# Kernel optimization log

Measured on AMD Instinct MI355X. Metric: run time of the kernel, lower is better.

The kernel has to match this reference:

```python
import jax, jax.numpy as jnp
import numpy as np

EPS = 1e-5
NUM_GROUPS = 32

def _nin(x, w, b):
    # 1x1 conv: x (B,C,H,W), w (K,C), b (K,)
    return jnp.einsum('bchw,kc->bkhw', x, w) + b[None, :, None, None]

def _group_norm(x, gamma, beta, num_groups=NUM_GROUPS, eps=EPS):
    B, C, H, W = x.shape
    xg = x.reshape(B, num_groups, C // num_groups, H, W)
    mean = xg.mean(axis=(2, 3, 4), keepdims=True)
    var = xg.var(axis=(2, 3, 4), keepdims=True)
    xg = (xg - mean) * jax.lax.rsqrt(var + eps)
    x = xg.reshape(B, C, H, W)
    return x * gamma[None, :, None, None] + beta[None, :, None, None]

def setup_inputs() -> dict:
    key = jax.random.key(0)
    ks = jax.random.split(key, 10)
    B, C, H, W = 8, 512, 64, 64
    att = 512
    s = 0.02
    return {
        'x': jax.random.normal(ks[0], (B, C, H, W), dtype=jnp.float32),
        'gn_weight': jnp.ones((C,), jnp.float32),
        'gn_bias': jnp.zeros((C,), jnp.float32),
        'q_w': jax.random.normal(ks[1], (att, C), jnp.float32) * s,
        'q_b': jnp.zeros((att,), jnp.float32),
        'k_w': jax.random.normal(ks[2], (att, C), jnp.float32) * s,
        'k_b': jnp.zeros((att,), jnp.float32),
        'v_w': jax.random.normal(ks[3], (att, C), jnp.float32) * s,
        'v_b': jnp.zeros((att,), jnp.float32),
        'proj_w': jax.random.normal(ks[4], (C, att), jnp.float32) * s,
        'proj_b': jnp.zeros((C,), jnp.float32),
    }

def reference(x, gn_weight, gn_bias, q_w, q_b, k_w, k_b, v_w, v_b, proj_w, proj_b):
    B, C, H, W = x.shape
    h = _group_norm(x, gn_weight, gn_bias)
    q = _nin(h, q_w, q_b)  # (B, D, H, W)
    k = _nin(h, k_w, k_b)
    v = _nin(h, v_w, v_b)
    N = H * W
    qf = q.reshape(B, -1, N)
    kf = k.reshape(B, -1, N)
    vf = v.reshape(B, -1, N)
    scale = C ** (-0.5)  # note: scaled by input channel C, per source
    w = jnp.einsum('bdn,bdm->bnm', qf, kf) * scale  # (B, N, N)
    w = jax.nn.softmax(w, axis=-1)
    hf = jnp.einsum('bnm,bdm->bdn', w, vf)
    h = hf.reshape(B, -1, H, W)
    h = _nin(h, proj_w, proj_b)
    return x + h
```

## Files before the change

kernel.cpp:

```cpp
#include <hip/hip_runtime.h>
#include <hip/hip_bf16.h>
#include <cstdint>
#include <cstddef>

typedef __bf16 bf16_t;
typedef __bf16 bf16x8 __attribute__((ext_vector_type(8)));
typedef __bf16 bf16x4 __attribute__((ext_vector_type(4)));
typedef float f32x4 __attribute__((ext_vector_type(4)));

__device__ __forceinline__ void async16(const void* g, void* l) {
  __builtin_amdgcn_global_load_lds(
      (const __attribute__((address_space(1))) void*)g,
      (__attribute__((address_space(3))) void*)l,
      16, 0, 0);
}

__global__ __launch_bounds__(256) void f2b4(const float* __restrict__ w0,
                                            const float* __restrict__ w1,
                                            const float* __restrict__ w2,
                                            const float* __restrict__ w3,
                                            bf16_t* __restrict__ o0,
                                            bf16_t* __restrict__ o1,
                                            bf16_t* __restrict__ o2,
                                            bf16_t* __restrict__ o3) {
  const float* in = (blockIdx.y == 0) ? w0 : (blockIdx.y == 1) ? w1
                   : (blockIdx.y == 2) ? w2 : w3;
  bf16_t* out = (blockIdx.y == 0) ? o0 : (blockIdx.y == 1) ? o1
               : (blockIdx.y == 2) ? o2 : o3;
  const int i = blockIdx.x * 256 + threadIdx.x;
  float4 v = ((const float4*)in)[i];
  bf16x4 o = { (__bf16)v.x, (__bf16)v.y, (__bf16)v.z, (__bf16)v.w };
  ((bf16x4*)out)[i] = o;
}

__global__ __launch_bounds__(256) void groupnorm_t(const float* __restrict__ x,
                                                   const float* __restrict__ gamma,
                                                   const float* __restrict__ beta,
                                                   bf16_t* __restrict__ ht) {
  const int g = blockIdx.x;
  const int b = blockIdx.y;
  const int t = threadIdx.x;
  const float* xg = x + ((size_t)(b * 512 + g * 16)) * 4096;
  const float4* x4 = (const float4*)xg;

  float s = 0.f, ss = 0.f;
  #pragma unroll 8
  for (int i = t; i < 16384; i += 256) {
    float4 v = x4[i];
    s  += (v.x + v.y) + (v.z + v.w);
    ss += (v.x * v.x + v.y * v.y) + (v.z * v.z + v.w * v.w);
  }
  #pragma unroll
  for (int o = 32; o; o >>= 1) { s += __shfl_xor(s, o); ss += __shfl_xor(ss, o); }
  __shared__ float rs[4], rss[4];
  if ((t & 63) == 0) { rs[t >> 6] = s; rss[t >> 6] = ss; }
  __syncthreads();
  const float S  = (rs[0] + rs[1]) + (rs[2] + rs[3]);
  const float SS = (rss[0] + rss[1]) + (rss[2] + rss[3]);
  const float inv_n = 1.0f / 65536.0f;
  const float mean = S * inv_n;
  const float var  = SS * inv_n - mean * mean;
  const float rstd = rsqrtf(var + 1e-5f);

  float ga[16], be[16];
  #pragma unroll
  for (int cc = 0; cc < 16; cc++) {
    const float gm = gamma[g * 16 + cc] * rstd;
    ga[cc] = gm;
    be[cc] = beta[g * 16 + cc] - mean * gm;
  }

  bf16_t* hg = ht + (size_t)b * 4096 * 512 + g * 16;
  for (int n = t; n < 4096; n += 256) {
    bf16_t o[16];
    #pragma unroll
    for (int cc = 0; cc < 16; cc++)
      o[cc] = (bf16_t)(xg[(size_t)cc * 4096 + n] * ga[cc] + be[cc]);
    bf16x8* dst = (bf16x8*)(hg + (size_t)n * 512);
    dst[0] = *(bf16x8*)&o[0];
    dst[1] = *(bf16x8*)&o[8];
  }
}

template <int OUTF32, int BIAS_MODE, int RESID, int SWAP>
__global__ __launch_bounds__(256)
void gemm_bt(const bf16_t* __restrict__ A, const bf16_t* __restrict__ B,
             void* __restrict__ Cv, const float* __restrict__ bias,
             const float* __restrict__ resid,
             int TM, int TN, int Z, int K, float scale,
             long sA, long sB, long sC, long sR) {
  __shared__ alignas(16) bf16_t lA[4096];
  __shared__ alignas(16) bf16_t lB[4096];

  const int lid = blockIdx.x;
  const int xcd = lid & 7;
  const int j   = lid >> 3;
  const int sd  = SWAP ? TN : TM;
  const int I   = SWAP ? TM : TN;
  const int spx = (sd * Z) >> 3;
  const int strip = xcd * spx + j / I;
  const int inner = j % I;
  const int z    = strip / sd;
  const int sidx = strip % sd;
  const int bm = (SWAP ? inner : sidx) * 128;
  const int bn = (SWAP ? sidx : inner) * 128;
  const int N = TN * 128;

  const int t = threadIdx.x;
  const int lane = t & 63;
  const int w = t >> 6;
  const int wm = (w >> 1) * 64;
  const int wn = (w & 1) * 64;
  const bf16_t* Ab = A + (size_t)z * (size_t)sA;
  const bf16_t* Bb = B + (size_t)z * (size_t)sB;

  const int lrow = lane >> 2;
  const int lcol = (lane & 3) * 8;
  const int quad = lane >> 4;
  const int l15 = lane & 15;

  const bf16_t* gA0 = Ab + (size_t)(bm + w * 16 + lrow) * K + lcol;
  const bf16_t* gA1 = Ab + (size_t)(bm + (w + 4) * 16 + lrow) * K + lcol;
  const bf16_t* gB0 = Bb + (size_t)(bn + w * 16 + lrow) * K + lcol;
  const bf16_t* gB1 = Bb + (size_t)(bn + (w + 4) * 16 + lrow) * K + lcol;
  bf16_t* lA0 = &lA[w * 512];
  bf16_t* lA1 = &lA[(w + 4) * 512];
  bf16_t* lB0 = &lB[w * 512];
  bf16_t* lB1 = &lB[(w + 4) * 512];

  f32x4 acc[4][4] = {};

  for (int k0 = 0; k0 < K; k0 += 32) {
    __syncthreads();
    async16(gA0 + k0, lA0);
    async16(gA1 + k0, lA1);
    async16(gB0 + k0, lB0);
    async16(gB1 + k0, lB1);
    __syncthreads();

    bf16x8 af[4], bfr[4];
    #pragma unroll
    for (int i = 0; i < 4; i++) {
      af[i]  = *(const bf16x8*)&lA[(wm + i * 16 + l15) * 32 + quad * 8];
      bfr[i] = *(const bf16x8*)&lB[(wn + i * 16 + l15) * 32 + quad * 8];
    }
    #pragma unroll
    for (int i = 0; i < 4; i++)
      #pragma unroll
      for (int jj = 0; jj < 4; jj++)
        acc[i][jj] = __builtin_amdgcn_mfma_f32_16x16x32_bf16(af[i], bfr[jj],
                                                             acc[i][jj], 0, 0, 0);
  }

  float* Cf = (float*)Cv + (size_t)z * (size_t)sC;
  bf16_t* Cb = (bf16_t*)Cv + (size_t)z * (size_t)sC;
  const float* Rb = RESID ? (resid + (size_t)z * (size_t)sR) : nullptr;

  #pragma unroll
  for (int i = 0; i < 4; i++) {
    const int row0 = bm + wm + i * 16 + quad * 4;
    #pragma unroll
    for (int jj = 0; jj < 4; jj++) {
      const int col = bn + wn + jj * 16 + l15;
      #pragma unroll
      for (int r = 0; r < 4; r++) {
        float v = acc[i][jj][r] * scale;
        const int row = row0 + r;
        if (BIAS_MODE == 1) v += bias[row];
        else if (BIAS_MODE == 2) v += bias[col];
        const size_t idx = (size_t)row * N + col;
        if (RESID) v += Rb[idx];
        if (OUTF32) Cf[idx] = v;
        else Cb[idx] = (bf16_t)v;
      }
    }
  }
}

__global__ __launch_bounds__(256, 2)
void flash_attn(const bf16_t* __restrict__ Qm, const bf16_t* __restrict__ Km,
                const bf16_t* __restrict__ Vm, bf16_t* __restrict__ Om,
                float scale) {
  __shared__ alignas(16) bf16_t lT[4][128][32];
  __shared__ alignas(16) bf16_t lS[4][16][144];

  const int bid = blockIdx.x;
  const int z = bid & 7;
  const int qb = bid >> 3;
  const int m0 = qb * 64;

  const int t = threadIdx.x;
  const int lane = t & 63;
  const int w = t >> 6;
  const int quad = lane >> 4;
  const int l15 = lane & 15;
  const int srow = lane >> 2;
  const int scol = (lane & 3) * 8;

  const size_t sND = 4096ull * 512;
  const bf16_t* q = Qm + z * sND;
  const bf16_t* k = Km + z * sND;
  const bf16_t* v = Vm + z * sND;

  bf16x8 qf[16];
  {
    const bf16_t* qrow = q + (size_t)(m0 + w * 16 + l15) * 512 + quad * 8;
    #pragma unroll
    for (int kk = 0; kk < 16; kk++)
      qf[kk] = *(const bf16x8*)(qrow + kk * 32);
  }

  f32x4 o_acc[32] = {};
  float l_run[4] = {0.f, 0.f, 0.f, 0.f};

  for (int kc = 0; kc < 4096; kc += 128) {
    f32x4 s_acc[8] = {};
    #pragma unroll
    for (int kd2 = 0; kd2 < 4; kd2++) {
      __syncthreads();
      #pragma unroll
      for (int c = 0; c < 8; c++) {
        const int p = c >> 1;
        const int keyblk = w * 32 + (c & 1) * 16;
        const bf16_t* g = k + (size_t)(kc + keyblk + srow) * 512
                            + kd2 * 128 + p * 32 + scol;
        async16(g, &lT[p][keyblk][0] + srow * 32 + scol);
      }
      __syncthreads();
      #pragma unroll
      for (int p = 0; p < 4; p++)
        #pragma unroll
        for (int n = 0; n < 8; n++) {
          bf16x8 kf = *(const bf16x8*)&lT[p][n * 16 + l15][quad * 8];
          s_acc[n] = __builtin_amdgcn_mfma_f32_16x16x32_bf16(
              qf[kd2 * 4 + p], kf, s_acc[n], 0, 0, 0);
        }
    }

    float lsum[4] = {0.f, 0.f, 0.f, 0.f};
    #pragma unroll
    for (int n = 0; n < 8; n++)
      #pragma unroll
      for (int r = 0; r < 4; r++) {
        float e = __expf(s_acc[n][r] * scale);
        lsum[r] += e;
        lS[w][quad * 4 + r][n * 16 + l15] = (bf16_t)e;
      }
    #pragma unroll
    for (int r = 0; r < 4; r++) {
      float s = lsum[r];
      s += __shfl_xor(s, 1); s += __shfl_xor(s, 2);
      s += __shfl_xor(s, 4); s += __shfl_xor(s, 8);
      l_run[r] += s;
    }

    #pragma unroll
    for (int db = 0; db < 4; db++) {
      __syncthreads();
      #pragma unroll
      for (int c = 0; c < 8; c++) {
        const int p = c >> 1;
        const int dblk = w * 32 + (c & 1) * 16;
        const bf16_t* g = v + (size_t)(db * 128 + dblk + srow) * 4096
                            + kc + p * 32 + scol;
        async16(g, &lT[p][dblk][0] + srow * 32 + scol);
      }
      __syncthreads();
      #pragma unroll
      for (int p = 0; p < 4; p++) {
        bf16x8 af = *(const bf16x8*)&lS[w][l15][p * 32 + quad * 8];
        #pragma unroll
        for (int nd = 0; nd < 8; nd++) {
          bf16x8 vf = *(const bf16x8*)&lT[p][nd * 16 + l15][quad * 8];
          o_acc[db * 8 + nd] = __builtin_amdgcn_mfma_f32_16x16x32_bf16(
              af, vf, o_acc[db * 8 + nd], 0, 0, 0);
        }
      }
    }
  }

  bf16_t* o = Om + z * sND;
  float rl[4];
  #pragma unroll
  for (int r = 0; r < 4; r++) rl[r] = 1.0f / l_run[r];
  #pragma unroll
  for (int nd = 0; nd < 32; nd++)
    #pragma unroll
    for (int r = 0; r < 4; r++) {
      const int row = m0 + w * 16 + quad * 4 + r;
      const int col = nd * 16 + l15;
      o[(size_t)row * 512 + col] = (bf16_t)(o_acc[nd][r] * rl[r]);
    }
}

extern "C" void kernel_launch(void* const* d_in, const int* in_sizes, int n_in,
                              void* d_out, int out_size, void* d_ws, size_t ws_size,
                              hipStream_t stream) {
  const float* x   = (const float*)d_in[0];
  const float* gnw = (const float*)d_in[1];
  const float* gnb = (const float*)d_in[2];
  const float* qw  = (const float*)d_in[3];
  const float* qb  = (const float*)d_in[4];
  const float* kw  = (const float*)d_in[5];
  const float* kb  = (const float*)d_in[6];
  const float* vw  = (const float*)d_in[7];
  const float* vb  = (const float*)d_in[8];
  const float* pw  = (const float*)d_in[9];
  const float* pb  = (const float*)d_in[10];
  float* out = (float*)d_out;

  char* ws = (char*)d_ws;
  size_t off = 0;
  auto alloc = [&](size_t bytes) -> void* {
    void* p = ws + off;
    off += (bytes + 255) & ~(size_t)255;
    return p;
  };

  const long sND = 4096L * 512;

  bf16_t* wqb = (bf16_t*)alloc(512ull * 512 * 2);
  bf16_t* wkb = (bf16_t*)alloc(512ull * 512 * 2);
  bf16_t* wvb = (bf16_t*)alloc(512ull * 512 * 2);
  bf16_t* wpb = (bf16_t*)alloc(512ull * 512 * 2);
  bf16_t* ht  = (bf16_t*)alloc(8ull * 4096 * 512 * 2);
  bf16_t* qbf = (bf16_t*)alloc(8ull * 4096 * 512 * 2);
  bf16_t* kbf = (bf16_t*)alloc(8ull * 4096 * 512 * 2);
  bf16_t* vbf = (bf16_t*)alloc(8ull * 4096 * 512 * 2);
  bf16_t* hfb = ht;

  f2b4<<<dim3(256, 4), 256, 0, stream>>>(qw, kw, vw, pw, wqb, wkb, wvb, wpb);
  groupnorm_t<<<dim3(32, 8), 256, 0, stream>>>(x, gnw, gnb, ht);

  gemm_bt<0, 2, 0, 0><<<1024, 256, 0, stream>>>(
      ht, wqb, qbf, qb, nullptr, 32, 4, 8, 512, 1.0f, sND, 0, sND, 0);
  gemm_bt<0, 2, 0, 0><<<1024, 256, 0, stream>>>(
      ht, wkb, kbf, kb, nullptr, 32, 4, 8, 512, 1.0f, sND, 0, sND, 0);
  gemm_bt<0, 1, 0, 1><<<1024, 256, 0, stream>>>(
      wvb, ht, vbf, vb, nullptr, 4, 32, 8, 512, 1.0f, 0, sND, sND, 0);

  const float scale = 0.044194173824159216f;
  flash_attn<<<512, 256, 0, stream>>>(qbf, kbf, vbf, hfb, scale);

  gemm_bt<1, 1, 1, 1><<<1024, 256, 0, stream>>>(
      wpb, hfb, out, pb, x, 4, 32, 8, 512, 1.0f, 0, sND, 512L * 4096, 512L * 4096);
}
```

Measured before the change: 747.5 us.

## Double-buffer K/V tiles in flash attention with prefetch and swizzled LDS

Replaces the single LDS tile, which was loaded and then waited on before every MMA step, with a two-slot buffer. The next K or V slab is prefetched with async global-to-LDS loads while the current slab is consumed, and the prefetch continues across the K-to-V and V-to-next-K boundaries. It also stores tiles in fragment-native order so each lane reads contiguously, XOR-swizzles the probability tile to avoid bank conflicts, and raises wave priority around the MMA loops. The cost is twice the LDS footprint, which may reduce occupancy.

```diff
diff --git a/kernel.cpp b/kernel.cpp
--- a/kernel.cpp
+++ b/kernel.cpp
@@ -181,8 +181,8 @@
 void flash_attn(const bf16_t* __restrict__ Qm, const bf16_t* __restrict__ Km,
                 const bf16_t* __restrict__ Vm, bf16_t* __restrict__ Om,
                 float scale) {
-  __shared__ alignas(16) bf16_t lT[4][128][32];
-  __shared__ alignas(16) bf16_t lS[4][16][144];
+  __shared__ alignas(16) bf16_t lK[2][16384];
+  __shared__ alignas(16) bf16_t lS[4][2048];
 
   const int bid = blockIdx.x;
   const int z = bid & 7;
@@ -194,14 +194,15 @@
   const int w = t >> 6;
   const int quad = lane >> 4;
   const int l15 = lane & 15;
-  const int srow = lane >> 2;
-  const int scol = (lane & 3) * 8;
 
   const size_t sND = 4096ull * 512;
   const bf16_t* q = Qm + z * sND;
   const bf16_t* k = Km + z * sND;
   const bf16_t* v = Vm + z * sND;
 
+  const int kOffK = l15 * 512 + quad * 8;
+  const int kOffV = l15 * 4096 + quad * 8;
+
   bf16x8 qf[16];
   {
     const bf16_t* qrow = q + (size_t)(m0 + w * 16 + l15) * 512 + quad * 8;
@@ -213,69 +214,102 @@
   f32x4 o_acc[32] = {};
   float l_run[4] = {0.f, 0.f, 0.f, 0.f};
 
+  #pragma unroll
+  for (int c = 0; c < 8; c++) {
+    const int p = c >> 1, n = (w << 1) | (c & 1);
+    async16(k + (size_t)(n * 16) * 512 + p * 32 + kOffK,
+            &lK[0][(p * 8 + n) << 9]);
+  }
+  __syncthreads();
+
   for (int kc = 0; kc < 4096; kc += 128) {
     f32x4 s_acc[8] = {};
+    float lsum[4] = {0.f, 0.f, 0.f, 0.f};
+
     #pragma unroll
     for (int kd2 = 0; kd2 < 4; kd2++) {
-      __syncthreads();
-      #pragma unroll
-      for (int c = 0; c < 8; c++) {
-        const int p = c >> 1;
-        const int keyblk = w * 32 + (c & 1) * 16;
-        const bf16_t* g = k + (size_t)(kc + keyblk + srow) * 512
-                            + kd2 * 128 + p * 32 + scol;
-        async16(g, &lT[p][keyblk][0] + srow * 32 + scol);
-      }
-      __syncthreads();
+      if (kd2 < 3) {
+        #pragma unroll
+        for (int c = 0; c < 8; c++) {
+          const int p = c >> 1, n = (w << 1) | (c & 1);
+          async16(k + (size_t)(kc + n * 16) * 512 + (kd2 + 1) * 128 + p * 32 + kOffK,
+                  &lK[(kd2 + 1) & 1][(p * 8 + n) << 9]);
+        }
+      } else {
+        #pragma unroll
+        for (int c = 0; c < 8; c++) {
+          const int p = c >> 1, nd = (w << 1) | (c & 1);
+          async16(v + (size_t)(nd * 16) * 4096 + kc + p * 32 + kOffV,
+                  &lK[(kd2 + 1) & 1][(p * 8 + nd) << 9]);
+        }
+      }
+      const bf16_t* buf = lK[kd2 & 1];
+      __builtin_amdgcn_s_setprio(1);
       #pragma unroll
       for (int p = 0; p < 4; p++)
         #pragma unroll
         for (int n = 0; n < 8; n++) {
-          bf16x8 kf = *(const bf16x8*)&lT[p][n * 16 + l15][quad * 8];
+          bf16x8 kf = *(const bf16x8*)&buf[((p * 8 + n) << 9) + lane * 8];
           s_acc[n] = __builtin_amdgcn_mfma_f32_16x16x32_bf16(
               qf[kd2 * 4 + p], kf, s_acc[n], 0, 0, 0);
         }
-    }
-
-    float lsum[4] = {0.f, 0.f, 0.f, 0.f};
-    #pragma unroll
-    for (int n = 0; n < 8; n++)
-      #pragma unroll
-      for (int r = 0; r < 4; r++) {
-        float e = __expf(s_acc[n][r] * scale);
-        lsum[r] += e;
-        lS[w][quad * 4 + r][n * 16 + l15] = (bf16_t)e;
-      }
-    #pragma unroll
-    for (int r = 0; r < 4; r++) {
-      float s = lsum[r];
-      s += __shfl_xor(s, 1); s += __shfl_xor(s, 2);
-      s += __shfl_xor(s, 4); s += __shfl_xor(s, 8);
-      l_run[r] += s;
+      __builtin_amdgcn_s_setprio(0);
+
+      if (kd2 == 3) {
+        #pragma unroll
+        for (int n = 0; n < 8; n++)
+          #pragma unroll
+          for (int r = 0; r < 4; r++) {
+            float e = __expf(s_acc[n][r] * scale);
+            lsum[r] += e;
+            const int row = quad * 4 + r;
+            const int sl = ((n * 2 + (l15 >> 3)) ^ row) & 15;
+            lS[w][row * 128 + sl * 8 + (l15 & 7)] = (bf16_t)e;
+          }
+        #pragma unroll
+        for (int r = 0; r < 4; r++) {
+          float s = lsum[r];
+          s += __shfl_xor(s, 1); s += __shfl_xor(s, 2);
+          s += __shfl_xor(s, 4); s += __shfl_xor(s, 8);
+          l_run[r] += s;
+        }
+      }
+      __syncthreads();
     }
 
     #pragma unroll
     for (int db = 0; db < 4; db++) {
-      __syncthreads();
-      #pragma unroll
-      for (int c = 0; c < 8; c++) {
-        const int p = c >> 1;
-        const int dblk = w * 32 + (c & 1) * 16;
-        const bf16_t* g = v + (size_t)(db * 128 + dblk + srow) * 4096
-                            + kc + p * 32 + scol;
-        async16(g, &lT[p][dblk][0] + srow * 32 + scol);
-      }
-      __syncthreads();
+      if (db < 3) {
+        #pragma unroll
+        for (int c = 0; c < 8; c++) {
+          const int p = c >> 1, nd = (w << 1) | (c & 1);
+          async16(v + (size_t)((db + 1) * 128 + nd * 16) * 4096 + kc + p * 32 + kOffV,
+                  &lK[(db + 1) & 1][(p * 8 + nd) << 9]);
+        }
+      } else {
+        const int kc2 = (kc + 128) & 4095;
+        #pragma unroll
+        for (int c = 0; c < 8; c++) {
+          const int p = c >> 1, n = (w << 1) | (c & 1);
+          async16(k + (size_t)(kc2 + n * 16) * 512 + p * 32 + kOffK,
+                  &lK[(db + 1) & 1][(p * 8 + n) << 9]);
+        }
+      }
+      const bf16_t* buf = lK[db & 1];
+      __builtin_amdgcn_s_setprio(1);
       #pragma unroll
       for (int p = 0; p < 4; p++) {
-        bf16x8 af = *(const bf16x8*)&lS[w][l15][p * 32 + quad * 8];
+        bf16x8 af = *(const bf16x8*)
+            &lS[w][l15 * 128 + (((p * 4 + quad) ^ l15) & 15) * 8];
         #pragma unroll
         for (int nd = 0; nd < 8; nd++) {
-          bf16x8 vf = *(const bf16x8*)&lT[p][nd * 16 + l15][quad * 8];
+          bf16x8 vf = *(const bf16x8*)&buf[((p * 8 + nd) << 9) + lane * 8];
           o_acc[db * 8 + nd] = __builtin_amdgcn_mfma_f32_16x16x32_bf16(
               af, vf, o_acc[db * 8 + nd], 0, 0, 0);
         }
       }
+      __builtin_amdgcn_s_setprio(0);
+      __syncthreads();
     }
   }
 
```

After: 958.9 us. +28.3%, slower.

## Store K/V tiles in MFMA fragment order, swizzle P buffer, raise MFMA priority

Applied to the files above, without the earlier changes.

Rewrites the LDS layout of the K and V tiles so each async 16-byte load lands exactly where a lane later reads its MFMA operand, making the LDS reads contiguous per lane and free of bank conflicts. Adds an XOR swizzle to the probability (P) scratch buffer to remove bank conflicts on its writes and reads. Wraps the MFMA loops in s_setprio so compute waves get scheduling priority. The global load pattern changes to per-lane rows of 16 bytes, which may coalesce less well across lanes.

```diff
diff --git a/kernel.cpp b/kernel.cpp
--- a/kernel.cpp
+++ b/kernel.cpp
@@ -181,8 +181,8 @@
 void flash_attn(const bf16_t* __restrict__ Qm, const bf16_t* __restrict__ Km,
                 const bf16_t* __restrict__ Vm, bf16_t* __restrict__ Om,
                 float scale) {
-  __shared__ alignas(16) bf16_t lT[4][128][32];
-  __shared__ alignas(16) bf16_t lS[4][16][144];
+  __shared__ alignas(16) bf16_t lT[32][512];
+  __shared__ alignas(16) bf16_t lS[4][2048];
 
   const int bid = blockIdx.x;
   const int z = bid & 7;
@@ -194,14 +194,15 @@
   const int w = t >> 6;
   const int quad = lane >> 4;
   const int l15 = lane & 15;
-  const int srow = lane >> 2;
-  const int scol = (lane & 3) * 8;
 
   const size_t sND = 4096ull * 512;
   const bf16_t* q = Qm + z * sND;
   const bf16_t* k = Km + z * sND;
   const bf16_t* v = Vm + z * sND;
 
+  const int kOffK = l15 * 512 + quad * 8;
+  const int kOffV = l15 * 4096 + quad * 8;
+
   bf16x8 qf[16];
   {
     const bf16_t* qrow = q + (size_t)(m0 + w * 16 + l15) * 512 + quad * 8;
@@ -221,20 +222,21 @@
       #pragma unroll
       for (int c = 0; c < 8; c++) {
         const int p = c >> 1;
-        const int keyblk = w * 32 + (c & 1) * 16;
-        const bf16_t* g = k + (size_t)(kc + keyblk + srow) * 512
-                            + kd2 * 128 + p * 32 + scol;
-        async16(g, &lT[p][keyblk][0] + srow * 32 + scol);
+        const int n = (w << 1) | (c & 1);
+        async16(k + (size_t)(kc + n * 16) * 512 + kd2 * 128 + p * 32 + kOffK,
+                &lT[p * 8 + n][0]);
       }
       __syncthreads();
+      __builtin_amdgcn_s_setprio(1);
       #pragma unroll
       for (int p = 0; p < 4; p++)
         #pragma unroll
         for (int n = 0; n < 8; n++) {
-          bf16x8 kf = *(const bf16x8*)&lT[p][n * 16 + l15][quad * 8];
+          bf16x8 kf = *(const bf16x8*)&lT[p * 8 + n][lane * 8];
           s_acc[n] = __builtin_amdgcn_mfma_f32_16x16x32_bf16(
               qf[kd2 * 4 + p], kf, s_acc[n], 0, 0, 0);
         }
+      __builtin_amdgcn_s_setprio(0);
     }
 
     float lsum[4] = {0.f, 0.f, 0.f, 0.f};
@@ -244,7 +246,9 @@
       for (int r = 0; r < 4; r++) {
         float e = __expf(s_acc[n][r] * scale);
         lsum[r] += e;
-        lS[w][quad * 4 + r][n * 16 + l15] = (bf16_t)e;
+        const int row = quad * 4 + r;
+        const int sl = ((n * 2 + (l15 >> 3)) ^ row) & 15;
+        lS[w][row * 128 + sl * 8 + (l15 & 7)] = (bf16_t)e;
       }
     #pragma unroll
     for (int r = 0; r < 4; r++) {
@@ -260,22 +264,24 @@
       #pragma unroll
       for (int c = 0; c < 8; c++) {
         const int p = c >> 1;
-        const int dblk = w * 32 + (c & 1) * 16;
-        const bf16_t* g = v + (size_t)(db * 128 + dblk + srow) * 4096
-                            + kc + p * 32 + scol;
-        async16(g, &lT[p][dblk][0] + srow * 32 + scol);
+        const int nd = (w << 1) | (c & 1);
+        async16(v + (size_t)(db * 128 + nd * 16) * 4096 + kc + p * 32 + kOffV,
+                &lT[p * 8 + nd][0]);
       }
       __syncthreads();
+      __builtin_amdgcn_s_setprio(1);
       #pragma unroll
       for (int p = 0; p < 4; p++) {
-        bf16x8 af = *(const bf16x8*)&lS[w][l15][p * 32 + quad * 8];
+        bf16x8 af = *(const bf16x8*)
+            &lS[w][l15 * 128 + (((p * 4 + quad) ^ l15) & 15) * 8];
         #pragma unroll
         for (int nd = 0; nd < 8; nd++) {
-          bf16x8 vf = *(const bf16x8*)&lT[p][nd * 16 + l15][quad * 8];
+          bf16x8 vf = *(const bf16x8*)&lT[p * 8 + nd][lane * 8];
           o_acc[db * 8 + nd] = __builtin_amdgcn_mfma_f32_16x16x32_bf16(
               af, vf, o_acc[db * 8 + nd], 0, 0, 0);
         }
       }
+      __builtin_amdgcn_s_setprio(0);
     }
   }
 
```

Result: slower. 890.7 us (+19.2%).

## Double-buffer K/V staging and widen flash attention blocks to 8 waves

Applied to the files above, without the earlier changes.

Flash attention now uses 512-thread blocks covering 128 query rows, so each staged K/V tile in shared memory is shared by twice as many waves. K and V tiles are double-buffered: the next tile's async global-to-LDS load is issued before the MFMA work on the current buffer, leaving one barrier per stage instead of two. This is meant to hide load latency and cut global traffic per query. In exchange it uses more LDS per block and fewer blocks in total (256), which may affect occupancy and load balance across CUs.

```diff
diff --git a/kernel.cpp b/kernel.cpp
--- a/kernel.cpp
+++ b/kernel.cpp
@@ -177,17 +177,17 @@
   }
 }
 
-__global__ __launch_bounds__(256, 2)
+__global__ __launch_bounds__(512, 2)
 void flash_attn(const bf16_t* __restrict__ Qm, const bf16_t* __restrict__ Km,
                 const bf16_t* __restrict__ Vm, bf16_t* __restrict__ Om,
                 float scale) {
-  __shared__ alignas(16) bf16_t lT[4][128][32];
-  __shared__ alignas(16) bf16_t lS[4][16][144];
+  __shared__ alignas(16) bf16_t lT[2][4][128][32];
+  __shared__ alignas(16) bf16_t lS[8][16][144];
 
   const int bid = blockIdx.x;
   const int z = bid & 7;
   const int qb = bid >> 3;
-  const int m0 = qb * 64;
+  const int m0 = qb * 128;
 
   const int t = threadIdx.x;
   const int lane = t & 63;
@@ -202,6 +202,9 @@
   const bf16_t* k = Km + z * sND;
   const bf16_t* v = Vm + z * sND;
 
+  const bf16_t* kStage = k + (size_t)(w * 16 + srow) * 512 + scol;
+  const bf16_t* vStage = v + (size_t)(w * 16 + srow) * 4096 + scol;
+
   bf16x8 qf[16];
   {
     const bf16_t* qrow = q + (size_t)(m0 + w * 16 + l15) * 512 + quad * 8;
@@ -212,31 +215,43 @@
 
   f32x4 o_acc[32] = {};
   float l_run[4] = {0.f, 0.f, 0.f, 0.f};
-
-  for (int kc = 0; kc < 4096; kc += 128) {
-    f32x4 s_acc[8] = {};
-    #pragma unroll
-    for (int kd2 = 0; kd2 < 4; kd2++) {
-      __syncthreads();
-      #pragma unroll
-      for (int c = 0; c < 8; c++) {
-        const int p = c >> 1;
-        const int keyblk = w * 32 + (c & 1) * 16;
-        const bf16_t* g = k + (size_t)(kc + keyblk + srow) * 512
-                            + kd2 * 128 + p * 32 + scol;
-        async16(g, &lT[p][keyblk][0] + srow * 32 + scol);
+  f32x4 s_acc[8];
+
+  auto stageA = [&](int BUF, int kcc, int kd2) __attribute__((always_inline)) {
+    #pragma unroll
+    for (int c = 0; c < 4; c++)
+      async16(kStage + (size_t)kcc * 512 + kd2 * 128 + c * 32,
+              &lT[BUF][c][w * 16][0]);
+  };
+  auto stageC = [&](int BUF, int kcc, int db) __attribute__((always_inline)) {
+    #pragma unroll
+    for (int c = 0; c < 4; c++)
+      async16(vStage + (size_t)db * 128 * 4096 + kcc + c * 32,
+              &lT[BUF][c][w * 16][0]);
+  };
+  auto computeA = [&](int BUF, int kd2) __attribute__((always_inline)) {
+    #pragma unroll
+    for (int p = 0; p < 4; p++)
+      #pragma unroll
+      for (int n = 0; n < 8; n++) {
+        bf16x8 kf = *(const bf16x8*)&lT[BUF][p][n * 16 + l15][quad * 8];
+        s_acc[n] = __builtin_amdgcn_mfma_f32_16x16x32_bf16(
+            qf[kd2 * 4 + p], kf, s_acc[n], 0, 0, 0);
       }
-      __syncthreads();
-      #pragma unroll
-      for (int p = 0; p < 4; p++)
-        #pragma unroll
-        for (int n = 0; n < 8; n++) {
-          bf16x8 kf = *(const bf16x8*)&lT[p][n * 16 + l15][quad * 8];
-          s_acc[n] = __builtin_amdgcn_mfma_f32_16x16x32_bf16(
-              qf[kd2 * 4 + p], kf, s_acc[n], 0, 0, 0);
-        }
-    }
-
+  };
+  auto computeC = [&](int BUF, int db) __attribute__((always_inline)) {
+    #pragma unroll
+    for (int p = 0; p < 4; p++) {
+      bf16x8 af = *(const bf16x8*)&lS[w][l15][p * 32 + quad * 8];
+      #pragma unroll
+      for (int nd = 0; nd < 8; nd++) {
+        bf16x8 vf = *(const bf16x8*)&lT[BUF][p][nd * 16 + l15][quad * 8];
+        o_acc[db * 8 + nd] = __builtin_amdgcn_mfma_f32_16x16x32_bf16(
+            af, vf, o_acc[db * 8 + nd], 0, 0, 0);
+      }
+    }
+  };
+  auto phaseB = [&]() __attribute__((always_inline)) {
     float lsum[4] = {0.f, 0.f, 0.f, 0.f};
     #pragma unroll
     for (int n = 0; n < 8; n++)
@@ -253,30 +268,24 @@
       s += __shfl_xor(s, 4); s += __shfl_xor(s, 8);
       l_run[r] += s;
     }
-
-    #pragma unroll
-    for (int db = 0; db < 4; db++) {
-      __syncthreads();
-      #pragma unroll
-      for (int c = 0; c < 8; c++) {
-        const int p = c >> 1;
-        const int dblk = w * 32 + (c & 1) * 16;
-        const bf16_t* g = v + (size_t)(db * 128 + dblk + srow) * 4096
-                            + kc + p * 32 + scol;
-        async16(g, &lT[p][dblk][0] + srow * 32 + scol);
-      }
-      __syncthreads();
-      #pragma unroll
-      for (int p = 0; p < 4; p++) {
-        bf16x8 af = *(const bf16x8*)&lS[w][l15][p * 32 + quad * 8];
-        #pragma unroll
-        for (int nd = 0; nd < 8; nd++) {
-          bf16x8 vf = *(const bf16x8*)&lT[p][nd * 16 + l15][quad * 8];
-          o_acc[db * 8 + nd] = __builtin_amdgcn_mfma_f32_16x16x32_bf16(
-              af, vf, o_acc[db * 8 + nd], 0, 0, 0);
-        }
-      }
-    }
+  };
+
+  stageA(0, 0, 0);
+  __syncthreads();
+
+  for (int kc = 0; kc < 4096; kc += 128) {
+    #pragma unroll
+    for (int n = 0; n < 8; n++) s_acc[n] = (f32x4){0.f, 0.f, 0.f, 0.f};
+
+    stageA(1, kc, 1);  computeA(0, 0);            __syncthreads();
+    stageA(0, kc, 2);  computeA(1, 1);            __syncthreads();
+    stageA(1, kc, 3);  computeA(0, 2);            __syncthreads();
+    stageC(0, kc, 0);  computeA(1, 3);  phaseB(); __syncthreads();
+    stageC(1, kc, 1);  computeC(0, 0);            __syncthreads();
+    stageC(0, kc, 2);  computeC(1, 1);            __syncthreads();
+    stageC(1, kc, 3);  computeC(0, 2);            __syncthreads();
+    if (kc + 128 < 4096) stageA(0, kc + 128, 0);
+    computeC(1, 3);                               __syncthreads();
   }
 
   bf16_t* o = Om + z * sND;
@@ -340,7 +349,7 @@
       wvb, ht, vbf, vb, nullptr, 4, 32, 8, 512, 1.0f, 0, sND, sND, 0);
 
   const float scale = 0.044194173824159216f;
-  flash_attn<<<512, 256, 0, stream>>>(qbf, kbf, vbf, hfb, scale);
+  flash_attn<<<256, 512, 0, stream>>>(qbf, kbf, vbf, hfb, scale);
 
   gemm_bt<1, 1, 1, 1><<<1024, 256, 0, stream>>>(
       wpb, hfb, out, pb, x, 4, 32, 8, 512, 1.0f, 0, sND, 512L * 4096, 512L * 4096);
```

Result: faster. 701.8 us (-6.1%).
